# Performance work log

Hardware: AMD Instinct MI355X
Metric: run time of the kernel (lower is better)

The kernel has to match this reference:

```python
import jax, jax.numpy as jnp
import numpy as np

B, D, H, O, E, TOP_K = 1024, 1024, 2048, 1024, 8, 2


def setup_inputs() -> dict:
    key = jax.random.key(0)
    ks = jax.random.split(key, 8)
    s = 0.02
    return {
        "x":  jax.random.normal(ks[0], (B, D), dtype=jnp.float32),
        "Wr": jax.random.normal(ks[1], (D, E), dtype=jnp.float32) * s,
        "br": jnp.zeros((E,), dtype=jnp.float32),
        "W1": jax.random.normal(ks[2], (E, D, H), dtype=jnp.float32) * s,
        "b1": jnp.zeros((E, H), dtype=jnp.float32),
        "W2": jax.random.normal(ks[3], (E, H, H), dtype=jnp.float32) * s,
        "b2": jnp.zeros((E, H), dtype=jnp.float32),
        "W3": jax.random.normal(ks[4], (E, H, O), dtype=jnp.float32) * s,
        "b3": jnp.zeros((E, O), dtype=jnp.float32),
    }


def reference(x, Wr, br, W1, b1, W2, b2, W3, b3):
    # --- router: softmax -> top-k -> renormalize selected weights ---
    logits = x @ Wr + br                      # [B, E]
    probs = jax.nn.softmax(logits, axis=-1)
    w, ids = jax.lax.top_k(probs, TOP_K)      # [B, K], [B, K]
    w = w / (jnp.sum(w, axis=-1, keepdims=True) + 1e-6)

    # --- expert MLPs (depth=2: in->h, relu, h->h, relu, h->out) ---
    h = jax.nn.relu(jnp.einsum('bd,edh->beh', x, W1) + b1)   # [B, E, H]
    h = jax.nn.relu(jnp.einsum('beh,ehg->beg', h, W2) + b2)  # [B, E, H]
    y_e = jnp.einsum('beg,ego->beo', h, W3) + b3             # [B, E, O]

    # --- weighted scatter-combine: comb[b,e] = sum_k w[b,k] * [ids[b,k]==e] ---
    comb = jnp.sum(jax.nn.one_hot(ids, E, dtype=x.dtype) * w[..., None], axis=1)  # [B, E]
    out = jnp.einsum('beo,be->bo', y_e, comb)                # [B, O]
    return out
```

## Files before the change

### kernel.cpp

```cpp
#include <hip/hip_runtime.h>
#include <hip/hip_bf16.h>

#define BT 1024
#define DD 1024
#define HH 2048
#define OO 1024
#define EE 8
#define RMAX 3072

typedef __bf16 bf16x8 __attribute__((ext_vector_type(8)));
typedef float  f32x4  __attribute__((ext_vector_type(4)));

__device__ __forceinline__ void cp16(void* l, const void* g) {
    __builtin_amdgcn_global_load_lds(
        (const __attribute__((address_space(1))) void*)g,
        (__attribute__((address_space(3))) void*)l, 16, 0, 0);
}

#define VMW(n)  asm volatile("s_waitcnt vmcnt(" #n ")" ::: "memory")
#define LGKM(n) asm volatile("s_waitcnt lgkmcnt(" #n ")" ::: "memory")
#define SCHED0  __builtin_amdgcn_sched_barrier(0)
#define BAR()   __builtin_amdgcn_s_barrier()


__global__ __launch_bounds__(256) void router_kernel(
    const float* __restrict__ x, const float* __restrict__ Wr, const float* __restrict__ br,
    int* __restrict__ counts, int* __restrict__ elist,
    int* __restrict__ tok_e, int* __restrict__ tok_p, float* __restrict__ tok_w)
{
    int b = blockIdx.x;
    int tid = threadIdx.x;
    float acc[EE];
#pragma unroll
    for (int e = 0; e < EE; ++e) acc[e] = 0.f;
    const float* xr = x + (size_t)b * DD;
    for (int d = tid; d < DD; d += 256) {
        float xv = xr[d];
#pragma unroll
        for (int e = 0; e < EE; ++e) acc[e] += xv * Wr[d * EE + e];
    }
    __shared__ float red[4][EE];
    int lane = tid & 63, wv = tid >> 6;
#pragma unroll
    for (int e = 0; e < EE; ++e) {
        float v = acc[e];
#pragma unroll
        for (int o = 32; o > 0; o >>= 1) v += __shfl_down(v, o, 64);
        if (lane == 0) red[wv][e] = v;
    }
    __syncthreads();
    if (tid == 0) {
        float lg[EE];
#pragma unroll
        for (int e = 0; e < EE; ++e) lg[e] = red[0][e] + red[1][e] + red[2][e] + red[3][e] + br[e];
        float mx = lg[0];
#pragma unroll
        for (int e = 1; e < EE; ++e) mx = fmaxf(mx, lg[e]);
        float s = 0.f, p[EE];
#pragma unroll
        for (int e = 0; e < EE; ++e) { p[e] = expf(lg[e] - mx); s += p[e]; }
        float inv = 1.f / s;
#pragma unroll
        for (int e = 0; e < EE; ++e) p[e] *= inv;
        int i0 = 0; float b0 = p[0];
#pragma unroll
        for (int e = 1; e < EE; ++e) if (p[e] > b0) { b0 = p[e]; i0 = e; }
        int i1 = -1; float b1v = -1.f;
#pragma unroll
        for (int e = 0; e < EE; ++e) if (e != i0 && p[e] > b1v) { b1v = p[e]; i1 = e; }
        float s2 = b0 + b1v + 1e-6f;
        float w0 = b0 / s2, w1 = b1v / s2;
        int p0 = atomicAdd(&counts[i0], 1);
        int p1 = atomicAdd(&counts[i1], 1);
        elist[i0 * 1024 + p0] = b;
        elist[i1 * 1024 + p1] = b;
        tok_e[2 * b] = i0; tok_e[2 * b + 1] = i1;
        tok_p[2 * b] = p0; tok_p[2 * b + 1] = p1;
        tok_w[2 * b] = w0; tok_w[2 * b + 1] = w1;
    }
}

__global__ void offsets_kernel(const int* __restrict__ counts, int* __restrict__ off)
{
    if (threadIdx.x == 0 && blockIdx.x == 0) {
        int a = 0;
        for (int e = 0; e < EE; ++e) {
            off[e] = a;
            a += ((counts[e] + 127) >> 7) << 7;
        }
        off[EE] = a;
    }
}

__global__ __launch_bounds__(256) void gather_kernel(
    const float* __restrict__ x, const int* __restrict__ counts, const int* __restrict__ off,
    const int* __restrict__ elist, __bf16* __restrict__ Xg)
{
    int e = blockIdx.y;
    int chunk = blockIdx.x >> 2;
    int rg = blockIdx.x & 3;
    int cnt = counts[e];
    if (chunk * 128 >= cnt) return;
    int base = off[e] + chunk * 128 + rg * 32;
    int tid = threadIdx.x;
    for (int it = 0; it < 32; ++it) {
        int slot = chunk * 128 + rg * 32 + it;
        __bf16 v[4];
        if (slot < cnt) {
            int tok = elist[e * 1024 + slot];
            const float4 f = *(const float4*)(x + (size_t)tok * DD + tid * 4);
            v[0] = (__bf16)f.x; v[1] = (__bf16)f.y; v[2] = (__bf16)f.z; v[3] = (__bf16)f.w;
        } else {
            v[0] = v[1] = v[2] = v[3] = (__bf16)0.f;
        }
        *(uint2*)(Xg + (size_t)(base + it) * DD + tid * 4) = *(uint2*)v;
    }
}

template <int K, int N>
__global__ __launch_bounds__(512, 1) void wprep(const float* __restrict__ W, __bf16* __restrict__ Wb)
{
    int kb = blockIdx.x, e = blockIdx.y;
    int t = threadIdx.x;
    const float* Wp = W + (size_t)e * K * N + (size_t)kb * 32 * N;
    __shared__ __bf16 T[32 * N];

#pragma unroll
    for (int j = 0; j < N / 64; ++j) {
        int g = j * 512 + t;
        int row = g >> (N == 2048 ? 9 : 8);
        int n4 = g & (N / 4 - 1);
        float4 f = *(const float4*)(Wp + (size_t)row * N + n4 * 4);
        __bf16 v[4] = { (__bf16)f.x, (__bf16)f.y, (__bf16)f.z, (__bf16)f.w };
        *(uint2*)(&T[row * N + n4 * 4]) = *(uint2*)v;
    }
    __syncthreads();

    __bf16* Wbp = Wb + (((size_t)e * (N / 64)) * (K / 32) + kb) * 2048;
#pragma unroll
    for (int rnd = 0; rnd < (N / 64) * 256 / 512; ++rnd) {
        int c = rnd * 512 + t;
        int nt = c >> 8;
        int cid = c & 255;
        int n = cid >> 2, slot = cid & 3;
        int q = slot ^ ((n >> 1) & 3);
        __bf16 v[8];
#pragma unroll
        for (int kk = 0; kk < 8; ++kk)
            v[kk] = T[(q * 8 + kk) * N + nt * 64 + n];
        __bf16* dst = Wbp + (size_t)nt * (K / 32) * 2048 + n * 32 + slot * 8;
        *(uint4*)dst = *(uint4*)v;
    }
}

template <int K, int N, bool RELU, bool OUT_BF16>
__global__ __launch_bounds__(256, 3) void gemm_fused(
    const __bf16* __restrict__ A, const __bf16* __restrict__ Wb,
    const float* __restrict__ bias, void* __restrict__ OutV,
    const int* __restrict__ counts, const int* __restrict__ off)
{
    constexpr int NSTEPS = K / 32;

    int e  = blockIdx.x & 7;
    int nt = blockIdx.x >> 3;
    int mt = blockIdx.y;
    int cnt = counts[e];
    if (mt * 128 >= cnt) return;
    int row0 = off[e] + mt * 128;

    const __bf16* Ab = A + (size_t)row0 * K;
    const __bf16* Bp = Wb + ((size_t)e * (N / 64) + nt) * (size_t)(K / 32) * 2048;

    __shared__ __bf16 As[4 * 4096];
    __shared__ __bf16 Bs[4 * 2048];

    int tid = threadIdx.x;
    int wave = tid >> 6, lane = tid & 63;
    int m = lane & 15, q = lane >> 4;
    int wm = (wave >> 1) * 64, wn = (wave & 1) * 32;

    int adr = lane >> 2;
    int asrc = ((lane & 3) ^ ((lane >> 3) & 3)) * 8;

    f32x4 acc[4][2] = {};

    auto issue = [&](int t) {
        unsigned ab = (unsigned)(t & 3) * 4096;
        unsigned bb = (unsigned)(t & 3) * 2048;
        int s0 = wave * 32, s1 = wave * 32 + 16;
        cp16(&As[ab + wave * 1024 + lane * 8],
             Ab + (size_t)(s0 + adr) * K + t * 32 + asrc);
        cp16(&As[ab + wave * 1024 + 512 + lane * 8],
             Ab + (size_t)(s1 + adr) * K + t * 32 + asrc);
        cp16(&Bs[bb + wave * 512 + lane * 8],
             Bp + (size_t)t * 2048 + wave * 512 + lane * 8);
    };

    issue(0); issue(1); issue(2);

    for (int t = 0; t < NSTEPS; ++t) {
        if (t + 3 < NSTEPS) { VMW(6); } else { VMW(0); }
        SCHED0;
        BAR();
        SCHED0;
        if (t + 3 < NSTEPS) issue(t + 3);

        unsigned aR = (unsigned)(t & 3) * 4096;
        unsigned bR = (unsigned)(t & 3) * 2048;
        bf16x8 af[4], bfr[2];
#pragma unroll
        for (int i = 0; i < 4; ++i) {
            int row = wm + i * 16 + m;
            af[i] = *(bf16x8*)(&As[aR + row * 32 + (q ^ ((row >> 1) & 3)) * 8]);
        }
#pragma unroll
        for (int j = 0; j < 2; ++j) {
            int n = wn + j * 16 + m;
            bfr[j] = *(bf16x8*)(&Bs[bR + n * 32 + (q ^ ((n >> 1) & 3)) * 8]);
        }
        LGKM(0); SCHED0;
        __builtin_amdgcn_s_setprio(1);
#pragma unroll
        for (int i = 0; i < 4; ++i)
#pragma unroll
            for (int j = 0; j < 2; ++j)
                acc[i][j] = __builtin_amdgcn_mfma_f32_16x16x32_bf16(af[i], bfr[j], acc[i][j], 0, 0, 0);
        __builtin_amdgcn_s_setprio(0);
    }

    const float* bp = bias + (size_t)e * N;
    int colbase = nt * 64 + wn;
#pragma unroll
    for (int j = 0; j < 2; ++j) {
        int col = colbase + j * 16 + m;
        float bv = bp[col];
#pragma unroll
        for (int i = 0; i < 4; ++i) {
            int rbase = row0 + wm + i * 16 + q * 4;
#pragma unroll
            for (int r = 0; r < 4; ++r) {
                float v = acc[i][j][r] + bv;
                if constexpr (RELU) v = fmaxf(v, 0.f);
                if constexpr (OUT_BF16)
                    ((__bf16*)OutV)[(size_t)(rbase + r) * N + col] = (__bf16)v;
                else
                    ((float*)OutV)[(size_t)(rbase + r) * N + col] = v;
            }
        }
    }
}

__global__ __launch_bounds__(256) void combine_kernel(
    const float* __restrict__ Y, const int* __restrict__ off,
    const int* __restrict__ tok_e, const int* __restrict__ tok_p,
    const float* __restrict__ tok_w, float* __restrict__ out)
{
    int b = blockIdx.x, t = threadIdx.x;
    int e0 = tok_e[2 * b], e1 = tok_e[2 * b + 1];
    int r0 = off[e0] + tok_p[2 * b];
    int r1 = off[e1] + tok_p[2 * b + 1];
    float w0 = tok_w[2 * b], w1 = tok_w[2 * b + 1];
    int col = t * 4;
    f32x4 s0 = *(const f32x4*)(Y + (size_t)r0 * OO + col);
    f32x4 s1 = *(const f32x4*)(Y + (size_t)r1 * OO + col);
    f32x4 o = s0 * w0 + s1 * w1;
    *(f32x4*)(out + (size_t)b * OO + col) = o;
}

extern "C" void kernel_launch(void* const* d_in, const int* in_sizes, int n_in,
                              void* d_out, int out_size, void* d_ws, size_t ws_size,
                              hipStream_t stream)
{
    (void)in_sizes; (void)n_in; (void)out_size; (void)ws_size;
    const float* x  = (const float*)d_in[0];
    const float* Wr = (const float*)d_in[1];
    const float* br = (const float*)d_in[2];
    const float* W1 = (const float*)d_in[3];
    const float* b1 = (const float*)d_in[4];
    const float* W2 = (const float*)d_in[5];
    const float* b2 = (const float*)d_in[6];
    const float* W3 = (const float*)d_in[7];
    const float* b3 = (const float*)d_in[8];
    float* out = (float*)d_out;

    char* ws = (char*)d_ws;
    int*    counts = (int*)(ws + 0);
    int*    off    = (int*)(ws + 256);
    int*    tok_e  = (int*)(ws + 1024);
    int*    tok_p  = (int*)(ws + 9216);
    float*  tok_w  = (float*)(ws + 17408);
    int*    elist  = (int*)(ws + 25600);
    __bf16* Xg     = (__bf16*)(ws + 65536);
    __bf16* H1     = (__bf16*)(ws + 6356992);
    __bf16* H2     = (__bf16*)(ws + 18939904);
    float*  Y      = (float*)(ws + 31522816);
    __bf16* Wb1    = (__bf16*)(ws + 44105728);
    __bf16* Wb2    = (__bf16*)(ws + 77660160);
    __bf16* Wb3    = (__bf16*)(ws + 144769024);

    hipMemsetAsync(counts, 0, 256, stream);
    router_kernel<<<1024, 256, 0, stream>>>(x, Wr, br, counts, elist, tok_e, tok_p, tok_w);
    offsets_kernel<<<1, 64, 0, stream>>>(counts, off);
    gather_kernel<<<dim3(32, 8), 256, 0, stream>>>(x, counts, off, elist, Xg);

    wprep<1024, 2048><<<dim3(32, 8), 512, 0, stream>>>(W1, Wb1);
    wprep<2048, 2048><<<dim3(64, 8), 512, 0, stream>>>(W2, Wb2);
    wprep<2048, 1024><<<dim3(64, 8), 512, 0, stream>>>(W3, Wb3);

    gemm_fused<1024, 2048, true,  true ><<<dim3(256, 8), 256, 0, stream>>>(Xg, Wb1, b1, (void*)H1, counts, off);
    gemm_fused<2048, 2048, true,  true ><<<dim3(256, 8), 256, 0, stream>>>(H1, Wb2, b2, (void*)H2, counts, off);
    gemm_fused<2048, 1024, false, false><<<dim3(128, 8), 256, 0, stream>>>(H2, Wb3, b3, (void*)Y,  counts, off);

    combine_kernel<<<1024, 256, 0, stream>>>(Y, off, tok_e, tok_p, tok_w, out);
}
```

Baseline: 495.9 us.

## Fuse fp32 weight conversion into expert GEMMs, dropping separate wprep kernels

Removes the three weight-preprocessing kernels that converted fp32 expert weights to swizzled bf16 in workspace. Each GEMM now loads fp32 weights into registers, converts them, and writes them into a double-buffered LDS tile, using a two-step unrolled pipeline alongside the async A loads. This saves the extra write and re-read of the bf16 weight copies and three kernel launches. In exchange, each GEMM reads twice as many weight bytes through scalar strided loads, uses more registers, and launch bounds drop from 3 to 2 blocks per CU.

```diff
diff --git a/kernel.cpp b/kernel.cpp
--- a/kernel.cpp
+++ b/kernel.cpp
@@ -117,45 +117,9 @@
     }
 }
 
-template <int K, int N>
-__global__ __launch_bounds__(512, 1) void wprep(const float* __restrict__ W, __bf16* __restrict__ Wb)
-{
-    int kb = blockIdx.x, e = blockIdx.y;
-    int t = threadIdx.x;
-    const float* Wp = W + (size_t)e * K * N + (size_t)kb * 32 * N;
-    __shared__ __bf16 T[32 * N];
-
-#pragma unroll
-    for (int j = 0; j < N / 64; ++j) {
-        int g = j * 512 + t;
-        int row = g >> (N == 2048 ? 9 : 8);
-        int n4 = g & (N / 4 - 1);
-        float4 f = *(const float4*)(Wp + (size_t)row * N + n4 * 4);
-        __bf16 v[4] = { (__bf16)f.x, (__bf16)f.y, (__bf16)f.z, (__bf16)f.w };
-        *(uint2*)(&T[row * N + n4 * 4]) = *(uint2*)v;
-    }
-    __syncthreads();
-
-    __bf16* Wbp = Wb + (((size_t)e * (N / 64)) * (K / 32) + kb) * 2048;
-#pragma unroll
-    for (int rnd = 0; rnd < (N / 64) * 256 / 512; ++rnd) {
-        int c = rnd * 512 + t;
-        int nt = c >> 8;
-        int cid = c & 255;
-        int n = cid >> 2, slot = cid & 3;
-        int q = slot ^ ((n >> 1) & 3);
-        __bf16 v[8];
-#pragma unroll
-        for (int kk = 0; kk < 8; ++kk)
-            v[kk] = T[(q * 8 + kk) * N + nt * 64 + n];
-        __bf16* dst = Wbp + (size_t)nt * (K / 32) * 2048 + n * 32 + slot * 8;
-        *(uint4*)dst = *(uint4*)v;
-    }
-}
-
 template <int K, int N, bool RELU, bool OUT_BF16>
-__global__ __launch_bounds__(256, 3) void gemm_fused(
-    const __bf16* __restrict__ A, const __bf16* __restrict__ Wb,
+__global__ __launch_bounds__(256, 2) void gemm_fused(
+    const __bf16* __restrict__ A, const float* __restrict__ W,
     const float* __restrict__ bias, void* __restrict__ OutV,
     const int* __restrict__ counts, const int* __restrict__ off)
 {
@@ -169,44 +133,48 @@
     int row0 = off[e] + mt * 128;
 
     const __bf16* Ab = A + (size_t)row0 * K;
-    const __bf16* Bp = Wb + ((size_t)e * (N / 64) + nt) * (size_t)(K / 32) * 2048;
+    const float*  Wp = W + (size_t)e * K * N + nt * 64;
 
     __shared__ __bf16 As[4 * 4096];
-    __shared__ __bf16 Bs[4 * 2048];
+    __shared__ __bf16 Bs[2 * 2048];
 
     int tid = threadIdx.x;
     int wave = tid >> 6, lane = tid & 63;
     int m = lane & 15, q = lane >> 4;
     int wm = (wave >> 1) * 64, wn = (wave & 1) * 32;
 
-    int adr = lane >> 2;
+    int adr  = lane >> 2;
     int asrc = ((lane & 3) ^ ((lane >> 3) & 3)) * 8;
 
+    int bn = tid & 63;
+    int bkc = (tid >> 6) * 8;
+    int bslot = (bkc >> 3) ^ ((bn >> 1) & 3);
+
+    float bA[8], bB[8];
     f32x4 acc[4][2] = {};
 
-    auto issue = [&](int t) {
+    auto issueA = [&](int t) {
         unsigned ab = (unsigned)(t & 3) * 4096;
-        unsigned bb = (unsigned)(t & 3) * 2048;
-        int s0 = wave * 32, s1 = wave * 32 + 16;
         cp16(&As[ab + wave * 1024 + lane * 8],
-             Ab + (size_t)(s0 + adr) * K + t * 32 + asrc);
+             Ab + (size_t)(wave * 32 + adr) * K + t * 32 + asrc);
         cp16(&As[ab + wave * 1024 + 512 + lane * 8],
-             Ab + (size_t)(s1 + adr) * K + t * 32 + asrc);
-        cp16(&Bs[bb + wave * 512 + lane * 8],
-             Bp + (size_t)t * 2048 + wave * 512 + lane * 8);
+             Ab + (size_t)(wave * 32 + 16 + adr) * K + t * 32 + asrc);
     };
-
-    issue(0); issue(1); issue(2);
-
-    for (int t = 0; t < NSTEPS; ++t) {
-        if (t + 3 < NSTEPS) { VMW(6); } else { VMW(0); }
-        SCHED0;
-        BAR();
-        SCHED0;
-        if (t + 3 < NSTEPS) issue(t + 3);
-
+    auto loadB = [&](int t, float (&br_)[8]) {
+        const float* p = Wp + (size_t)(t * 32 + bkc) * N + bn;
+#pragma unroll
+        for (int g = 0; g < 8; ++g) br_[g] = p[(size_t)g * N];
+    };
+    auto writeB = [&](int tw, float (&br_)[8]) {
+        __attribute__((aligned(16))) __bf16 t8[8];
+#pragma unroll
+        for (int g = 0; g < 8; ++g) t8[g] = (__bf16)br_[g];
+        *(uint4*)(&Bs[(unsigned)(tw & 1) * 2048 + bn * 32 + bslot * 8]) = *(uint4*)t8;
+    };
+
+    auto compute = [&](int t) {
         unsigned aR = (unsigned)(t & 3) * 4096;
-        unsigned bR = (unsigned)(t & 3) * 2048;
+        unsigned bR = (unsigned)(t & 1) * 2048;
         bf16x8 af[4], bfr[2];
 #pragma unroll
         for (int i = 0; i < 4; ++i) {
@@ -226,6 +194,42 @@
             for (int j = 0; j < 2; ++j)
                 acc[i][j] = __builtin_amdgcn_mfma_f32_16x16x32_bf16(af[i], bfr[j], acc[i][j], 0, 0, 0);
         __builtin_amdgcn_s_setprio(0);
+    };
+
+    issueA(0);
+    loadB(0, bA);
+    issueA(1);
+    loadB(1, bB);
+    issueA(2);
+    VMW(12); SCHED0;
+    writeB(0, bA);
+    LGKM(0);
+
+    for (int t = 0; t < NSTEPS; t += 2) {
+        BAR(); SCHED0;
+        if (t + 3 < NSTEPS) issueA(t + 3);
+        if (t + 2 < NSTEPS) loadB(t + 2, bA);
+        SCHED0;
+        compute(t);
+        if (t < NSTEPS - 3)      { VMW(10); }
+        else                     { VMW(0);  }
+        SCHED0;
+        writeB(t + 1, bB);
+        LGKM(0);
+
+        BAR(); SCHED0;
+        if (t + 4 < NSTEPS) issueA(t + 4);
+        if (t + 3 < NSTEPS) loadB(t + 3, bB);
+        SCHED0;
+        compute(t + 1);
+        if (t + 1 < NSTEPS - 1) {
+            if (t + 1 < NSTEPS - 3)       { VMW(10); }
+            else if (t + 1 == NSTEPS - 3) { VMW(8);  }
+            else                          { VMW(0);  }
+            SCHED0;
+            writeB(t + 2, bA);
+            LGKM(0);
+        }
     }
 
     const float* bp = bias + (size_t)e * N;
@@ -294,22 +298,15 @@
     __bf16* H1     = (__bf16*)(ws + 6356992);
     __bf16* H2     = (__bf16*)(ws + 18939904);
     float*  Y      = (float*)(ws + 31522816);
-    __bf16* Wb1    = (__bf16*)(ws + 44105728);
-    __bf16* Wb2    = (__bf16*)(ws + 77660160);
-    __bf16* Wb3    = (__bf16*)(ws + 144769024);
 
     hipMemsetAsync(counts, 0, 256, stream);
     router_kernel<<<1024, 256, 0, stream>>>(x, Wr, br, counts, elist, tok_e, tok_p, tok_w);
     offsets_kernel<<<1, 64, 0, stream>>>(counts, off);
     gather_kernel<<<dim3(32, 8), 256, 0, stream>>>(x, counts, off, elist, Xg);
 
-    wprep<1024, 2048><<<dim3(32, 8), 512, 0, stream>>>(W1, Wb1);
-    wprep<2048, 2048><<<dim3(64, 8), 512, 0, stream>>>(W2, Wb2);
-    wprep<2048, 1024><<<dim3(64, 8), 512, 0, stream>>>(W3, Wb3);
-
-    gemm_fused<1024, 2048, true,  true ><<<dim3(256, 8), 256, 0, stream>>>(Xg, Wb1, b1, (void*)H1, counts, off);
-    gemm_fused<2048, 2048, true,  true ><<<dim3(256, 8), 256, 0, stream>>>(H1, Wb2, b2, (void*)H2, counts, off);
-    gemm_fused<2048, 1024, false, false><<<dim3(128, 8), 256, 0, stream>>>(H2, Wb3, b3, (void*)Y,  counts, off);
+    gemm_fused<1024, 2048, true,  true ><<<dim3(256, 8), 256, 0, stream>>>(Xg, W1, b1, (void*)H1, counts, off);
+    gemm_fused<2048, 2048, true,  true ><<<dim3(256, 8), 256, 0, stream>>>(H1, W2, b2, (void*)H2, counts, off);
+    gemm_fused<2048, 1024, false, false><<<dim3(128, 8), 256, 0, stream>>>(H2, W3, b3, (void*)Y,  counts, off);
 
     combine_kernel<<<1024, 256, 0, stream>>>(Y, off, tok_e, tok_p, tok_w, out);
 }
```

After: 420.7 us. 1.18x faster.
